# Kernel optimization log

Hardware: AMD Instinct MI355X
Metric: run time of the kernel (lower is better)

Reference implementation:

```python
import jax, jax.numpy as jnp
import numpy as np

B, T, D, U = 16, 1600, 512, 1024


def setup_inputs() -> dict:
    key = jax.random.key(0)
    ks = jax.random.split(key, 7)
    sk = 1.0 / np.sqrt(D)
    sr = 1.0 / np.sqrt(U)
    return {
        "x": jax.random.normal(ks[0], (B, T, D), jnp.float32),
        "x_len": jnp.full((B,), T, dtype=jnp.int32),
        "kernel_f": jax.random.normal(ks[1], (D, 4 * U), jnp.float32) * sk,
        "rkernel_f": jax.random.normal(ks[2], (U, 4 * U), jnp.float32) * sr,
        "bias_f": jnp.zeros((4 * U,), jnp.float32),
        "kernel_b": jax.random.normal(ks[3], (D, 4 * U), jnp.float32) * sk,
        "rkernel_b": jax.random.normal(ks[4], (U, 4 * U), jnp.float32) * sr,
        "bias_b": jnp.zeros((4 * U,), jnp.float32),
    }


def _lstm(x, kernel, rkernel, bias):
    """Keras-semantics LSTM, return_sequences=True. x: [B,T,D] -> [B,T,U]."""
    units = rkernel.shape[0]
    # precompute input projection for all timesteps (the big GEMM)
    xg = jnp.einsum('btd,dg->btg', x, kernel) + bias  # [B,T,4U]
    xg = jnp.swapaxes(xg, 0, 1)  # [T,B,4U] for scan
    h0 = jnp.zeros((x.shape[0], units), x.dtype)
    c0 = jnp.zeros((x.shape[0], units), x.dtype)

    def step(carry, g_in):
        h, c = carry
        g = g_in + h @ rkernel  # [B,4U]
        i, f, cc, o = jnp.split(g, 4, axis=-1)  # Keras gate order i,f,c,o
        c = jax.nn.sigmoid(f) * c + jax.nn.sigmoid(i) * jnp.tanh(cc)
        h = jax.nn.sigmoid(o) * jnp.tanh(c)
        return (h, c), h

    _, hs = jax.lax.scan(step, (h0, c0), xg)  # hs: [T,B,U]
    return jnp.swapaxes(hs, 0, 1)


def reference(x, x_len, kernel_f, rkernel_f, bias_f, kernel_b, rkernel_b, bias_b):
    # Bidirectional(LSTM(units, return_sequences=True)), merge_mode='concat'
    out_f = _lstm(x, kernel_f, rkernel_f, bias_f)
    out_b = _lstm(x[:, ::-1], kernel_b, rkernel_b, bias_b)[:, ::-1]
    outputs = jnp.concatenate([out_f, out_b], axis=-1)  # [B,T,2U]
    return outputs, x_len
```

## Files before the change

kernel.cpp:

```cpp
#include <hip/hip_runtime.h>

#define B_   16
#define T_   1600
#define D_   512
#define U_   1024
#define G_   4096
#define NWG  256
#define TPB  256
#define KTOT 1536
#define APAD 1544
#define ROWB (APAD*2)

typedef __attribute__((ext_vector_type(8))) __bf16 bf16x8;
typedef __attribute__((ext_vector_type(4))) float  f32x4;
typedef __attribute__((ext_vector_type(2))) float  f32x2;
typedef __attribute__((ext_vector_type(8))) unsigned short us8v;
typedef unsigned long long u64;

__device__ __forceinline__ unsigned short f2bf(float f) {
  unsigned u = __builtin_bit_cast(unsigned, f);
  u += 0x7FFFu + ((u >> 16) & 1u);
  return (unsigned short)(u >> 16);
}
__device__ __forceinline__ bf16x8 cvt8(const float4 a, const float4 b) {
  us8v r;
  r[0]=f2bf(a.x); r[1]=f2bf(a.y); r[2]=f2bf(a.z); r[3]=f2bf(a.w);
  r[4]=f2bf(b.x); r[5]=f2bf(b.y); r[6]=f2bf(b.z); r[7]=f2bf(b.w);
  return __builtin_bit_cast(bf16x8, r);
}
__device__ __forceinline__ float sigm(float x){ return 1.f / (1.f + __expf(-x)); }
__device__ __forceinline__ float tanh_(float x){ return 1.f - 2.f / (__expf(2.f*x) + 1.f); }

extern "C" __global__ void __launch_bounds__(TPB, 1)
bilstm_kernel(const float* __restrict__ x, const int* __restrict__ xlen,
              const float* __restrict__ kf, const float* __restrict__ rkf, const float* __restrict__ bf_,
              const float* __restrict__ kb, const float* __restrict__ rkb, const float* __restrict__ bb_,
              float* __restrict__ out, unsigned* __restrict__ flags,
              unsigned short* __restrict__ hbuf)
{
  extern __shared__ char smem[];

  const int tid = threadIdx.x;
  const int wg  = blockIdx.x;
  const int dir = wg >> 7;
  const int slot = wg & 127;
  const int u0  = slot << 3;

  if (wg == 0 && tid < B_)
    out[(size_t)B_*T_*2*U_ + tid] = (float)xlen[tid];

  const float* Km = dir ? kb  : kf;
  const float* Rm = dir ? rkb : rkf;
  const float* Bv = dir ? bb_ : bf_;

  const int w = tid >> 6, l = tid & 63;
  const int ntile = w & 1, khalf = w >> 1;

  {
    char* Wb = smem;
    for (int i = tid; i < KTOT*32; i += TPB) {
      int k = i >> 5, c = i & 31;
      int gc = ((c >> 3) << 10) + u0 + (c & 7);
      float wv = (k < D_) ? Km[(size_t)k*G_ + gc] : Rm[(size_t)(k-D_)*G_ + gc];
      *(unsigned short*)(Wb + c*ROWB + (k << 1)) = f2bf(wv);
    }
  }
  __syncthreads();

  bf16x8 wx[8], wh[16];
  {
    const char* Brow = smem + (ntile*16 + (l & 15))*ROWB + ((l >> 4) << 4);
    #pragma unroll
    for (int i = 0; i < 8; ++i)  wx[i] = *(const bf16x8*)(Brow + ((khalf*8 + i) << 6));
    #pragma unroll
    for (int i = 0; i < 16; ++i) wh[i] = *(const bf16x8*)(Brow + ((16 + khalf*16 + i) << 6));
  }
  __syncthreads();

  float* gates = (float*)smem;
  char*  hst   = smem + 4096;
  float* gp    = gates + khalf*512;
  const int drow0 = (l >> 4) << 2, dcol = ntile*16 + (l & 15);

  const int eb = tid >> 2, eup = (tid & 3) << 1;
  float bi0=0, bi1=0, bff0=0, bff1=0, bz0=0, bz1=0, bo0=0, bo1=0, c0=0, c1=0;
  if (tid < 64) {
    bi0 = Bv[u0+eup];        bi1 = Bv[u0+eup+1];
    bff0= Bv[1024+u0+eup];   bff1= Bv[1024+u0+eup+1];
    bz0 = Bv[2048+u0+eup];   bz1 = Bv[2048+u0+eup+1];
    bo0 = Bv[3072+u0+eup];   bo1 = Bv[3072+u0+eup+1];
  }

  unsigned* myflags = flags + dir*128;

  const float* xbase = x + (size_t)(l & 15)*T_*D_ + khalf*256 + ((l >> 4) << 3);

  const char* hrow  = hst + (l & 15)*2048;
  const int   kbase = (khalf*512 + ((l >> 4) << 3)) << 1;
  const int   swz   = ((l & 15) & 7) << 4;

  f32x4 acc = {0.f, 0.f, 0.f, 0.f};
  {
    const float* xA = xbase + (size_t)(dir ? (T_ - 1) : 0) * D_;
    #pragma unroll
    for (int i = 0; i < 8; ++i) {
      float4 lo = *(const float4*)(xA + i*32);
      float4 hi = *(const float4*)(xA + i*32 + 4);
      acc = __builtin_amdgcn_mfma_f32_16x16x32_bf16(cvt8(lo, hi), wx[i], acc, 0, 0, 0);
    }
  }

  for (int t = 0; t < T_; ++t) {
    const int tg = dir ? (T_ - 1 - t) : t;

    if (t > 0) {
      if (tid < 64) {
        const unsigned tgt = (unsigned)t;
        long long guard = 0;
        for (;;) {
          unsigned a = __hip_atomic_load(myflags + l,      __ATOMIC_RELAXED, __HIP_MEMORY_SCOPE_AGENT);
          unsigned b = __hip_atomic_load(myflags + 64 + l, __ATOMIC_RELAXED, __HIP_MEMORY_SCOPE_AGENT);
          if (__all((a >= tgt) && (b >= tgt))) break;
          __builtin_amdgcn_s_sleep(1);
          if (++guard > (1LL << 22)) break;
        }
      }
      __syncthreads();

      {
        const u64* hsrc = (const u64*)(hbuf + (((size_t)((t & 1)*2 + dir)) << 14));
        u64 tmp[16];
        #pragma unroll
        for (int j = 0; j < 16; ++j)
          tmp[j] = __hip_atomic_load(hsrc + tid + j*256, __ATOMIC_RELAXED, __HIP_MEMORY_SCOPE_AGENT);
        #pragma unroll
        for (int j = 0; j < 16; ++j)
          *(u64*)(hst + j*2048 + ((tid << 3) ^ ((j & 7) << 4))) = tmp[j];
      }
      __syncthreads();

      f32x4 acc2 = {0.f, 0.f, 0.f, 0.f};
      #pragma unroll
      for (int i = 0; i < 16; i += 2) {
        bf16x8 a0 = *(const bf16x8*)(hrow + ((kbase + i*64)       ^ swz));
        bf16x8 a1 = *(const bf16x8*)(hrow + ((kbase + (i+1)*64)   ^ swz));
        acc  = __builtin_amdgcn_mfma_f32_16x16x32_bf16(a0, wh[i],   acc,  0, 0, 0);
        acc2 = __builtin_amdgcn_mfma_f32_16x16x32_bf16(a1, wh[i+1], acc2, 0, 0, 0);
      }
      acc[0]+=acc2[0]; acc[1]+=acc2[1]; acc[2]+=acc2[2]; acc[3]+=acc2[3];
    }

    #pragma unroll
    for (int j = 0; j < 4; ++j) gp[(drow0 + j)*32 + dcol] = acc[j];
    __syncthreads();

    if (tid < 64) {
      const float* g0 = gates + eb*32 + eup;
      float gi0 = g0[0]  + g0[512] + bi0,  gi1 = g0[1]  + g0[513] + bi1;
      float gf0 = g0[8]  + g0[520] + bff0, gf1 = g0[9]  + g0[521] + bff1;
      float gz0 = g0[16] + g0[528] + bz0,  gz1 = g0[17] + g0[529] + bz1;
      float go0 = g0[24] + g0[536] + bo0,  go1 = g0[25] + g0[537] + bo1;
      c0 = sigm(gf0)*c0 + sigm(gi0)*tanh_(gz0);
      c1 = sigm(gf1)*c1 + sigm(gi1)*tanh_(gz1);
      float h0 = sigm(go0)*tanh_(c0);
      float h1 = sigm(go1)*tanh_(c1);
      f32x2 ho; ho.x = h0; ho.y = h1;
      __builtin_nontemporal_store(ho, (f32x2*)(out + ((size_t)eb*T_ + tg)*(2*U_) + (dir << 10) + u0 + eup));
      unsigned hp = ((unsigned)f2bf(h1) << 16) | (unsigned)f2bf(h0);
      unsigned* hdst = (unsigned*)(hbuf + (((size_t)(((t & 1) ^ 1)*2 + dir)) << 14) + (eb << 10) + u0 + eup);
      __hip_atomic_store(hdst, hp, __ATOMIC_RELAXED, __HIP_MEMORY_SCOPE_AGENT);
      asm volatile("s_waitcnt vmcnt(0)" ::: "memory");
      if (tid == 0)
        __hip_atomic_store(myflags + slot, (unsigned)(t + 1), __ATOMIC_RELAXED, __HIP_MEMORY_SCOPE_AGENT);
    }

    if (t + 1 < T_) {
      const float* xA = xbase + (size_t)(dir ? (T_ - 2 - t) : (t + 1)) * D_;
      f32x4 nacc = {0.f, 0.f, 0.f, 0.f};
      #pragma unroll
      for (int i = 0; i < 8; ++i) {
        float4 lo = *(const float4*)(xA + i*32);
        float4 hi = *(const float4*)(xA + i*32 + 4);
        nacc = __builtin_amdgcn_mfma_f32_16x16x32_bf16(cvt8(lo, hi), wx[i], nacc, 0, 0, 0);
      }
      acc = nacc;
    }
  }
}

extern "C" void kernel_launch(void* const* d_in, const int* in_sizes, int n_in,
                              void* d_out, int out_size, void* d_ws, size_t ws_size,
                              hipStream_t stream) {
  const float* x   = (const float*)d_in[0];
  const int*   xl  = (const int*)d_in[1];
  const float* kf  = (const float*)d_in[2];
  const float* rkf = (const float*)d_in[3];
  const float* bf_ = (const float*)d_in[4];
  const float* kb  = (const float*)d_in[5];
  const float* rkb = (const float*)d_in[6];
  const float* bb_ = (const float*)d_in[7];
  float* out = (float*)d_out;

  unsigned* flags = (unsigned*)d_ws;
  unsigned short* hbuf = (unsigned short*)((char*)d_ws + 1024);

  (void)hipMemsetAsync(d_ws, 0, 1024, stream);

  const size_t smem = 32*(size_t)ROWB;
  bilstm_kernel<<<NWG, TPB, smem, stream>>>(x, xl, kf, rkf, bf_, kb, rkb, bb_, out, flags, hbuf);
}
```

Baseline: 6.037 ms.

## Halve workgroup count with 16 units per block and stage x in LDS

```diff
diff --git a/kernel.cpp b/kernel.cpp
--- a/kernel.cpp
+++ b/kernel.cpp
@@ -5,11 +5,13 @@
 #define D_   512
 #define U_   1024
 #define G_   4096
-#define NWG  256
+#define NWG  128
 #define TPB  256
-#define KTOT 1536
-#define APAD 1544
-#define ROWB (APAD*2)
+#define WSTR 776
+#define GSTR 68
+#define XOFF 8704
+#define HOFF 25088
+#define SMEM_BYTES 99328
 
 typedef __attribute__((ext_vector_type(8))) __bf16 bf16x8;
 typedef __attribute__((ext_vector_type(4))) float  f32x4;
@@ -30,6 +32,22 @@
 }
 __device__ __forceinline__ float sigm(float x){ return 1.f / (1.f + __expf(-x)); }
 __device__ __forceinline__ float tanh_(float x){ return 1.f - 2.f / (__expf(2.f*x) + 1.f); }
+
+__device__ __forceinline__ void stage_x(const float* __restrict__ x, int tg1,
+                                        char* sm, int l) {
+  const int sb  = l >> 2;
+  const int skb = (l & 3) << 3;
+  const float* xs = x + ((size_t)sb*T_ + tg1)*D_;
+  char* xd = sm + XOFF + sb*1024;
+  const int ssz = (sb & 7) << 4;
+  #pragma unroll
+  for (int j = 0; j < 16; ++j) {
+    int k = skb + j*32;
+    float4 v0 = *(const float4*)(xs + k);
+    float4 v1 = *(const float4*)(xs + k + 4);
+    *(bf16x8*)(xd + ((k << 1) ^ ssz)) = cvt8(v0, v1);
+  }
+}
 
 extern "C" __global__ void __launch_bounds__(TPB, 1)
 bilstm_kernel(const float* __restrict__ x, const int* __restrict__ xlen,
@@ -40,11 +58,11 @@
 {
   extern __shared__ char smem[];
 
-  const int tid = threadIdx.x;
-  const int wg  = blockIdx.x;
-  const int dir = wg >> 7;
-  const int slot = wg & 127;
-  const int u0  = slot << 3;
+  const int tid  = threadIdx.x;
+  const int wg   = blockIdx.x;
+  const int dir  = wg >> 6;
+  const int slot = wg & 63;
+  const int u0   = slot << 4;
 
   if (wg == 0 && tid < B_)
     out[(size_t)B_*T_*2*U_ + tid] = (float)xlen[tid];
@@ -55,66 +73,75 @@
 
   const int w = tid >> 6, l = tid & 63;
   const int ntile = w & 1, khalf = w >> 1;
-
+  const int fr8 = (l >> 4) << 3;
+
+  bf16x8 wx[2][4], wh[2][8];
   {
-    char* Wb = smem;
-    for (int i = tid; i < KTOT*32; i += TPB) {
-      int k = i >> 5, c = i & 31;
-      int gc = ((c >> 3) << 10) + u0 + (c & 7);
-      float wv = (k < D_) ? Km[(size_t)k*G_ + gc] : Rm[(size_t)(k-D_)*G_ + gc];
-      *(unsigned short*)(Wb + c*ROWB + (k << 1)) = f2bf(wv);
-    }
-  }
+    unsigned short* stag = (unsigned short*)smem;
+    for (int half = 0; half < 2; ++half) {
+      for (int idx = tid; idx < 768*64; idx += TPB) {
+        int kl = idx >> 6, c = idx & 63;
+        int k = half*768 + kl;
+        int gc = (c & 3)*1024 + u0 + (c >> 2);
+        float wv = (k < D_) ? Km[(size_t)k*G_ + gc] : Rm[(size_t)(k-D_)*G_ + gc];
+        stag[c*WSTR + kl] = f2bf(wv);
+      }
+      __syncthreads();
+      #pragma unroll
+      for (int t2 = 0; t2 < 2; ++t2) {
+        int c = (ntile + t2*2)*16 + (l & 15);
+        if (half == 0) {
+          #pragma unroll
+          for (int i = 0; i < 4; ++i) {
+            int k = khalf*256 + i*64 + fr8;
+            wx[t2][i] = *(const bf16x8*)(stag + c*WSTR + k);
+          }
+        }
+        #pragma unroll
+        for (int i = 0; i < 8; ++i) {
+          int k = 512 + khalf*512 + i*64 + fr8;
+          int hf = (k >= 768) ? 1 : 0;
+          if (hf == half)
+            wh[t2][i] = *(const bf16x8*)(stag + c*WSTR + (k - half*768));
+        }
+      }
+      __syncthreads();
+    }
+  }
+
+  float* gates = (float*)smem;
+
+  const int eb  = (w & 1)*8 + (l >> 3);
+  const int eul = (l & 7) << 1;
+  float bias[8];
+  float cs0 = 0.f, cs1 = 0.f;
+  if (w < 2) {
+    #pragma unroll
+    for (int g = 0; g < 4; ++g) {
+      bias[g]     = Bv[g*1024 + u0 + eul];
+      bias[4 + g] = Bv[g*1024 + u0 + eul + 1];
+    }
+  }
+
+  unsigned* myflags = flags + dir*128;
+
+  const int r = l & 15;
+  const char* xr = smem + XOFF + r*1024;
+  const char* hr = smem + HOFF + r*2048;
+  const int sz = (r & 7) << 4;
+  const int c0 = ntile*16 + (l & 15);
+  const int c1 = c0 + 32;
+  const int drow0 = (l >> 4) << 2;
+  float* gp = gates + khalf*(16*GSTR);
+
+  if (w == 3) stage_x(x, dir ? (T_ - 1) : 0, smem, l);
   __syncthreads();
-
-  bf16x8 wx[8], wh[16];
-  {
-    const char* Brow = smem + (ntile*16 + (l & 15))*ROWB + ((l >> 4) << 4);
-    #pragma unroll
-    for (int i = 0; i < 8; ++i)  wx[i] = *(const bf16x8*)(Brow + ((khalf*8 + i) << 6));
-    #pragma unroll
-    for (int i = 0; i < 16; ++i) wh[i] = *(const bf16x8*)(Brow + ((16 + khalf*16 + i) << 6));
-  }
-  __syncthreads();
-
-  float* gates = (float*)smem;
-  char*  hst   = smem + 4096;
-  float* gp    = gates + khalf*512;
-  const int drow0 = (l >> 4) << 2, dcol = ntile*16 + (l & 15);
-
-  const int eb = tid >> 2, eup = (tid & 3) << 1;
-  float bi0=0, bi1=0, bff0=0, bff1=0, bz0=0, bz1=0, bo0=0, bo1=0, c0=0, c1=0;
-  if (tid < 64) {
-    bi0 = Bv[u0+eup];        bi1 = Bv[u0+eup+1];
-    bff0= Bv[1024+u0+eup];   bff1= Bv[1024+u0+eup+1];
-    bz0 = Bv[2048+u0+eup];   bz1 = Bv[2048+u0+eup+1];
-    bo0 = Bv[3072+u0+eup];   bo1 = Bv[3072+u0+eup+1];
-  }
-
-  unsigned* myflags = flags + dir*128;
-
-  const float* xbase = x + (size_t)(l & 15)*T_*D_ + khalf*256 + ((l >> 4) << 3);
-
-  const char* hrow  = hst + (l & 15)*2048;
-  const int   kbase = (khalf*512 + ((l >> 4) << 3)) << 1;
-  const int   swz   = ((l & 15) & 7) << 4;
-
-  f32x4 acc = {0.f, 0.f, 0.f, 0.f};
-  {
-    const float* xA = xbase + (size_t)(dir ? (T_ - 1) : 0) * D_;
-    #pragma unroll
-    for (int i = 0; i < 8; ++i) {
-      float4 lo = *(const float4*)(xA + i*32);
-      float4 hi = *(const float4*)(xA + i*32 + 4);
-      acc = __builtin_amdgcn_mfma_f32_16x16x32_bf16(cvt8(lo, hi), wx[i], acc, 0, 0, 0);
-    }
-  }
 
   for (int t = 0; t < T_; ++t) {
     const int tg = dir ? (T_ - 1 - t) : t;
 
     if (t > 0) {
-      if (tid < 64) {
+      if (w == 2) {
         const unsigned tgt = (unsigned)t;
         long long guard = 0;
         for (;;) {
@@ -128,62 +155,77 @@
       __syncthreads();
 
       {
-        const u64* hsrc = (const u64*)(hbuf + (((size_t)((t & 1)*2 + dir)) << 14));
+        const u64* hsrc = (const u64*)(hbuf + ((size_t)((t & 1)*2 + dir) << 14));
         u64 tmp[16];
         #pragma unroll
         for (int j = 0; j < 16; ++j)
           tmp[j] = __hip_atomic_load(hsrc + tid + j*256, __ATOMIC_RELAXED, __HIP_MEMORY_SCOPE_AGENT);
+        const int hb = (tid >> 2) & 15, hm = tid & 3, hs0 = tid >> 6;
+        char* hd = smem + HOFF + hb*2048;
+        const int hsz = (hb & 7) << 4;
         #pragma unroll
         for (int j = 0; j < 16; ++j)
-          *(u64*)(hst + j*2048 + ((tid << 3) ^ ((j & 7) << 4))) = tmp[j];
-      }
-      __syncthreads();
-
-      f32x4 acc2 = {0.f, 0.f, 0.f, 0.f};
+          *(u64*)(hd + (((hs0 + 4*j)*32 + hm*8) ^ hsz)) = tmp[j];
+      }
+      __syncthreads();
+    }
+
+    {
+      f32x4 aA = {0.f,0.f,0.f,0.f}, aB = aA, bA = aA, bB = aA;
       #pragma unroll
-      for (int i = 0; i < 16; i += 2) {
-        bf16x8 a0 = *(const bf16x8*)(hrow + ((kbase + i*64)       ^ swz));
-        bf16x8 a1 = *(const bf16x8*)(hrow + ((kbase + (i+1)*64)   ^ swz));
-        acc  = __builtin_amdgcn_mfma_f32_16x16x32_bf16(a0, wh[i],   acc,  0, 0, 0);
-        acc2 = __builtin_amdgcn_mfma_f32_16x16x32_bf16(a1, wh[i+1], acc2, 0, 0, 0);
-      }
-      acc[0]+=acc2[0]; acc[1]+=acc2[1]; acc[2]+=acc2[2]; acc[3]+=acc2[3];
-    }
-
-    #pragma unroll
-    for (int j = 0; j < 4; ++j) gp[(drow0 + j)*32 + dcol] = acc[j];
+      for (int i = 0; i < 4; ++i) {
+        bf16x8 av = *(const bf16x8*)(xr + (((khalf*256 + i*64 + fr8) << 1) ^ sz));
+        if (i & 1) { aB = __builtin_amdgcn_mfma_f32_16x16x32_bf16(av, wx[0][i], aB, 0,0,0);
+                     bB = __builtin_amdgcn_mfma_f32_16x16x32_bf16(av, wx[1][i], bB, 0,0,0); }
+        else       { aA = __builtin_amdgcn_mfma_f32_16x16x32_bf16(av, wx[0][i], aA, 0,0,0);
+                     bA = __builtin_amdgcn_mfma_f32_16x16x32_bf16(av, wx[1][i], bA, 0,0,0); }
+      }
+      if (t > 0) {
+        #pragma unroll
+        for (int i = 0; i < 8; ++i) {
+          bf16x8 av = *(const bf16x8*)(hr + (((khalf*512 + i*64 + fr8) << 1) ^ sz));
+          if (i & 1) { aB = __builtin_amdgcn_mfma_f32_16x16x32_bf16(av, wh[0][i], aB, 0,0,0);
+                       bB = __builtin_amdgcn_mfma_f32_16x16x32_bf16(av, wh[1][i], bB, 0,0,0); }
+          else       { aA = __builtin_amdgcn_mfma_f32_16x16x32_bf16(av, wh[0][i], aA, 0,0,0);
+                       bA = __builtin_amdgcn_mfma_f32_16x16x32_bf16(av, wh[1][i], bA, 0,0,0); }
+        }
+      }
+      aA += aB; bA += bB;
+      #pragma unroll
+      for (int j = 0; j < 4; ++j) {
+        gp[(drow0 + j)*GSTR + c0] = aA[j];
+        gp[(drow0 + j)*GSTR + c1] = bA[j];
+      }
+    }
     __syncthreads();
 
-    if (tid < 64) {
-      const float* g0 = gates + eb*32 + eup;
-      float gi0 = g0[0]  + g0[512] + bi0,  gi1 = g0[1]  + g0[513] + bi1;
-      float gf0 = g0[8]  + g0[520] + bff0, gf1 = g0[9]  + g0[521] + bff1;
-      float gz0 = g0[16] + g0[528] + bz0,  gz1 = g0[17] + g0[529] + bz1;
-      float go0 = g0[24] + g0[536] + bo0,  go1 = g0[25] + g0[537] + bo1;
-      c0 = sigm(gf0)*c0 + sigm(gi0)*tanh_(gz0);
-      c1 = sigm(gf1)*c1 + sigm(gi1)*tanh_(gz1);
-      float h0 = sigm(go0)*tanh_(c0);
-      float h1 = sigm(go1)*tanh_(c1);
-      f32x2 ho; ho.x = h0; ho.y = h1;
-      __builtin_nontemporal_store(ho, (f32x2*)(out + ((size_t)eb*T_ + tg)*(2*U_) + (dir << 10) + u0 + eup));
+    if (w < 2) {
+      const float* g0 = gates + eb*GSTR;
+      const float* g1 = gates + (16 + eb)*GSTR;
+      f32x4 u0a = *(const f32x4*)(g0 + eul*4);
+      f32x4 u0b = *(const f32x4*)(g1 + eul*4);
+      f32x4 u1a = *(const f32x4*)(g0 + eul*4 + 4);
+      f32x4 u1b = *(const f32x4*)(g1 + eul*4 + 4);
+      float gi0 = u0a[0]+u0b[0]+bias[0], gf0 = u0a[1]+u0b[1]+bias[1];
+      float gz0 = u0a[2]+u0b[2]+bias[2], go0 = u0a[3]+u0b[3]+bias[3];
+      float gi1 = u1a[0]+u1b[0]+bias[4], gf1 = u1a[1]+u1b[1]+bias[5];
+      float gz1 = u1a[2]+u1b[2]+bias[6], go1 = u1a[3]+u1b[3]+bias[7];
+      cs0 = sigm(gf0)*cs0 + sigm(gi0)*tanh_(gz0);
+      cs1 = sigm(gf1)*cs1 + sigm(gi1)*tanh_(gz1);
+      float h0 = sigm(go0)*tanh_(cs0);
+      float h1 = sigm(go1)*tanh_(cs1);
       unsigned hp = ((unsigned)f2bf(h1) << 16) | (unsigned)f2bf(h0);
-      unsigned* hdst = (unsigned*)(hbuf + (((size_t)(((t & 1) ^ 1)*2 + dir)) << 14) + (eb << 10) + u0 + eup);
+      unsigned* hdst = (unsigned*)(hbuf + ((size_t)(((t & 1) ^ 1)*2 + dir) << 14)
+                                   + slot*256 + eb*16 + eul);
       __hip_atomic_store(hdst, hp, __ATOMIC_RELAXED, __HIP_MEMORY_SCOPE_AGENT);
       asm volatile("s_waitcnt vmcnt(0)" ::: "memory");
-      if (tid == 0)
-        __hip_atomic_store(myflags + slot, (unsigned)(t + 1), __ATOMIC_RELAXED, __HIP_MEMORY_SCOPE_AGENT);
-    }
-
-    if (t + 1 < T_) {
-      const float* xA = xbase + (size_t)(dir ? (T_ - 2 - t) : (t + 1)) * D_;
-      f32x4 nacc = {0.f, 0.f, 0.f, 0.f};
-      #pragma unroll
-      for (int i = 0; i < 8; ++i) {
-        float4 lo = *(const float4*)(xA + i*32);
-        float4 hi = *(const float4*)(xA + i*32 + 4);
-        nacc = __builtin_amdgcn_mfma_f32_16x16x32_bf16(cvt8(lo, hi), wx[i], nacc, 0, 0, 0);
-      }
-      acc = nacc;
+      if (l == 0)
+        __hip_atomic_store(myflags + ((w & 1) ? 64 : 0) + slot, (unsigned)(t + 1),
+                           __ATOMIC_RELAXED, __HIP_MEMORY_SCOPE_AGENT);
+      f32x2 ho; ho.x = h0; ho.y = h1;
+      *(f32x2*)(out + ((size_t)eb*T_ + tg)*(2*U_) + (dir << 10) + u0 + eul) = ho;
+    } else if (w == 3 && t + 1 < T_) {
+      stage_x(x, dir ? (T_ - 2 - t) : (t + 1), smem, l);
     }
   }
 }
@@ -206,6 +248,6 @@
 
   (void)hipMemsetAsync(d_ws, 0, 1024, stream);
 
-  const size_t smem = 32*(size_t)ROWB;
-  bilstm_kernel<<<NWG, TPB, smem, stream>>>(x, xl, kf, rkf, bf_, kb, rkb, bb_, out, flags, hbuf);
-}
+  bilstm_kernel<<<NWG, TPB, SMEM_BYTES, stream>>>(x, xl, kf, rkf, bf_, kb, rkb, bb_,
+                                                  out, flags, hbuf);
+}
```

After: 12.00 ms. 98.7% more time.

## Pre-convert x to bf16, spread flag polling across all threads, defer output store

Applied to the files above, without the earlier changes.

```diff
diff --git a/kernel.cpp b/kernel.cpp
--- a/kernel.cpp
+++ b/kernel.cpp
@@ -10,6 +10,7 @@
 #define KTOT 1536
 #define APAD 1544
 #define ROWB (APAD*2)
+#define X16OFF (1 << 18)
 
 typedef __attribute__((ext_vector_type(8))) __bf16 bf16x8;
 typedef __attribute__((ext_vector_type(4))) float  f32x4;
@@ -31,12 +32,21 @@
 __device__ __forceinline__ float sigm(float x){ return 1.f / (1.f + __expf(-x)); }
 __device__ __forceinline__ float tanh_(float x){ return 1.f - 2.f / (__expf(2.f*x) + 1.f); }
 
+extern "C" __global__ void __launch_bounds__(256)
+xcvt_kernel(const float* __restrict__ xin, unsigned short* __restrict__ x16) {
+  const size_t i = ((size_t)blockIdx.x*256 + threadIdx.x) * 8;
+  float4 a = *(const float4*)(xin + i);
+  float4 b = *(const float4*)(xin + i + 4);
+  *(us8v*)(x16 + i) = __builtin_bit_cast(us8v, cvt8(a, b));
+}
+
 extern "C" __global__ void __launch_bounds__(TPB, 1)
 bilstm_kernel(const float* __restrict__ x, const int* __restrict__ xlen,
               const float* __restrict__ kf, const float* __restrict__ rkf, const float* __restrict__ bf_,
               const float* __restrict__ kb, const float* __restrict__ rkb, const float* __restrict__ bb_,
               float* __restrict__ out, unsigned* __restrict__ flags,
-              unsigned short* __restrict__ hbuf)
+              unsigned short* __restrict__ hbuf,
+              const unsigned short* __restrict__ x16, int use16)
 {
   extern __shared__ char smem[];
 
@@ -94,6 +104,7 @@
   unsigned* myflags = flags + dir*128;
 
   const float* xbase = x + (size_t)(l & 15)*T_*D_ + khalf*256 + ((l >> 4) << 3);
+  const unsigned short* x16b = x16 + (size_t)(l & 15)*T_*D_ + khalf*256 + ((l >> 4) << 3);
 
   const char* hrow  = hst + (l & 15)*2048;
   const int   kbase = (khalf*512 + ((l >> 4) << 3)) << 1;
@@ -101,12 +112,20 @@
 
   f32x4 acc = {0.f, 0.f, 0.f, 0.f};
   {
-    const float* xA = xbase + (size_t)(dir ? (T_ - 1) : 0) * D_;
-    #pragma unroll
-    for (int i = 0; i < 8; ++i) {
-      float4 lo = *(const float4*)(xA + i*32);
-      float4 hi = *(const float4*)(xA + i*32 + 4);
-      acc = __builtin_amdgcn_mfma_f32_16x16x32_bf16(cvt8(lo, hi), wx[i], acc, 0, 0, 0);
+    const int tg0 = dir ? (T_ - 1) : 0;
+    if (use16) {
+      const unsigned short* xA = x16b + (size_t)tg0 * D_;
+      #pragma unroll
+      for (int i = 0; i < 8; ++i)
+        acc = __builtin_amdgcn_mfma_f32_16x16x32_bf16(*(const bf16x8*)(xA + i*32), wx[i], acc, 0, 0, 0);
+    } else {
+      const float* xA = xbase + (size_t)tg0 * D_;
+      #pragma unroll
+      for (int i = 0; i < 8; ++i) {
+        float4 lo = *(const float4*)(xA + i*32);
+        float4 hi = *(const float4*)(xA + i*32 + 4);
+        acc = __builtin_amdgcn_mfma_f32_16x16x32_bf16(cvt8(lo, hi), wx[i], acc, 0, 0, 0);
+      }
     }
   }
 
@@ -114,19 +133,14 @@
     const int tg = dir ? (T_ - 1 - t) : t;
 
     if (t > 0) {
-      if (tid < 64) {
+      {
         const unsigned tgt = (unsigned)t;
         long long guard = 0;
-        for (;;) {
-          unsigned a = __hip_atomic_load(myflags + l,      __ATOMIC_RELAXED, __HIP_MEMORY_SCOPE_AGENT);
-          unsigned b = __hip_atomic_load(myflags + 64 + l, __ATOMIC_RELAXED, __HIP_MEMORY_SCOPE_AGENT);
-          if (__all((a >= tgt) && (b >= tgt))) break;
+        while (__hip_atomic_load(myflags + (tid >> 1), __ATOMIC_RELAXED, __HIP_MEMORY_SCOPE_AGENT) < tgt) {
           __builtin_amdgcn_s_sleep(1);
           if (++guard > (1LL << 22)) break;
         }
       }
-      __syncthreads();
-
       {
         const u64* hsrc = (const u64*)(hbuf + (((size_t)((t & 1)*2 + dir)) << 14));
         u64 tmp[16];
@@ -142,8 +156,8 @@
       f32x4 acc2 = {0.f, 0.f, 0.f, 0.f};
       #pragma unroll
       for (int i = 0; i < 16; i += 2) {
-        bf16x8 a0 = *(const bf16x8*)(hrow + ((kbase + i*64)       ^ swz));
-        bf16x8 a1 = *(const bf16x8*)(hrow + ((kbase + (i+1)*64)   ^ swz));
+        bf16x8 a0 = *(const bf16x8*)(hrow + ((kbase + i*64)     ^ swz));
+        bf16x8 a1 = *(const bf16x8*)(hrow + ((kbase + (i+1)*64) ^ swz));
         acc  = __builtin_amdgcn_mfma_f32_16x16x32_bf16(a0, wh[i],   acc,  0, 0, 0);
         acc2 = __builtin_amdgcn_mfma_f32_16x16x32_bf16(a1, wh[i+1], acc2, 0, 0, 0);
       }
@@ -164,24 +178,32 @@
       c1 = sigm(gf1)*c1 + sigm(gi1)*tanh_(gz1);
       float h0 = sigm(go0)*tanh_(c0);
       float h1 = sigm(go1)*tanh_(c1);
-      f32x2 ho; ho.x = h0; ho.y = h1;
-      __builtin_nontemporal_store(ho, (f32x2*)(out + ((size_t)eb*T_ + tg)*(2*U_) + (dir << 10) + u0 + eup));
       unsigned hp = ((unsigned)f2bf(h1) << 16) | (unsigned)f2bf(h0);
       unsigned* hdst = (unsigned*)(hbuf + (((size_t)(((t & 1) ^ 1)*2 + dir)) << 14) + (eb << 10) + u0 + eup);
       __hip_atomic_store(hdst, hp, __ATOMIC_RELAXED, __HIP_MEMORY_SCOPE_AGENT);
       asm volatile("s_waitcnt vmcnt(0)" ::: "memory");
       if (tid == 0)
         __hip_atomic_store(myflags + slot, (unsigned)(t + 1), __ATOMIC_RELAXED, __HIP_MEMORY_SCOPE_AGENT);
+      f32x2 ho; ho.x = h0; ho.y = h1;
+      *(f32x2*)(out + ((size_t)eb*T_ + tg)*(2*U_) + (dir << 10) + u0 + eup) = ho;
     }
 
     if (t + 1 < T_) {
-      const float* xA = xbase + (size_t)(dir ? (T_ - 2 - t) : (t + 1)) * D_;
+      const int tg1 = dir ? (T_ - 2 - t) : (t + 1);
       f32x4 nacc = {0.f, 0.f, 0.f, 0.f};
-      #pragma unroll
-      for (int i = 0; i < 8; ++i) {
-        float4 lo = *(const float4*)(xA + i*32);
-        float4 hi = *(const float4*)(xA + i*32 + 4);
-        nacc = __builtin_amdgcn_mfma_f32_16x16x32_bf16(cvt8(lo, hi), wx[i], nacc, 0, 0, 0);
+      if (use16) {
+        const unsigned short* xA = x16b + (size_t)tg1 * D_;
+        #pragma unroll
+        for (int i = 0; i < 8; ++i)
+          nacc = __builtin_amdgcn_mfma_f32_16x16x32_bf16(*(const bf16x8*)(xA + i*32), wx[i], nacc, 0, 0, 0);
+      } else {
+        const float* xA = xbase + (size_t)tg1 * D_;
+        #pragma unroll
+        for (int i = 0; i < 8; ++i) {
+          float4 lo = *(const float4*)(xA + i*32);
+          float4 hi = *(const float4*)(xA + i*32 + 4);
+          nacc = __builtin_amdgcn_mfma_f32_16x16x32_bf16(cvt8(lo, hi), wx[i], nacc, 0, 0, 0);
+        }
       }
       acc = nacc;
     }
@@ -203,9 +225,16 @@
 
   unsigned* flags = (unsigned*)d_ws;
   unsigned short* hbuf = (unsigned short*)((char*)d_ws + 1024);
+  unsigned short* x16  = (unsigned short*)((char*)d_ws + X16OFF);
+
+  const size_t need = (size_t)X16OFF + (size_t)B_*T_*D_*2;
+  const int use16 = (ws_size >= need) ? 1 : 0;
 
   (void)hipMemsetAsync(d_ws, 0, 1024, stream);
+  if (use16)
+    xcvt_kernel<<<6400, 256, 0, stream>>>(x, x16);
 
   const size_t smem = 32*(size_t)ROWB;
-  bilstm_kernel<<<NWG, TPB, smem, stream>>>(x, xl, kf, rkf, bf_, kb, rkb, bb_, out, flags, hbuf);
-}
+  bilstm_kernel<<<NWG, TPB, smem, stream>>>(x, xl, kf, rkf, bf_, kb, rkb, bb_,
+                                            out, flags, hbuf, x16, use16);
+}
```

After: 5.343 ms. -11.5%, faster.
